# Kernel tuning notes

Measured on AMD Instinct MI355X. Metric: run time of the kernel, lower is better.

The kernel has to match this reference:

```python
import jax, jax.numpy as jnp
import numpy as np

KH, KW = 2, 2  # kernel_size; stride == kernel_size (default), pad == 0 for this config

def setup_inputs() -> dict:
    key = jax.random.key(0)
    k1, k2 = jax.random.split(key)
    B, C, H, W = 32, 64, 64, 64
    nH, nW = H // KH, W // KW
    L = nH * nW                     # 1024
    n = KH * KW * C                 # 256 (grouping = in_feature)
    x = jax.random.normal(k1, (B, C, H, W), dtype=jnp.float32)
    stdv = 6.0 / np.sqrt(n * n / 1.0) ** 0.5  # placeholder, recomputed below
    stdv = 6.0 / np.sqrt(float(n * n) / 1.0) if False else 6.0 / np.sqrt(float(n) * float(n) / float(n)) / 1.0
    stdv = 6.0 / np.sqrt(float(n * n))  # numel // L == n*n -> stdv = 6/sqrt(n*n) = 6/n
    weight = jax.random.uniform(k2, (L, n, n), dtype=jnp.float32, minval=-stdv, maxval=stdv)
    bias = jnp.zeros((1, 1, n, L), dtype=jnp.float32)
    return {"x": x, "weight": weight, "bias": bias}

def reference(x, weight, bias):
    # PointConv with kernel=(2,2), stride=(2,2), pad=0, grouping=C.
    B, C, H, W = x.shape
    nH, nW = H // KH, W // KW
    L = nH * nW
    n = C * KH * KW
    # F.unfold (non-overlapping, stride==kernel): channel order (c, kh, kw), L order (ph, pw)
    patches = x.reshape(B, C, nH, KH, nW, KW).transpose(0, 1, 3, 5, 2, 4).reshape(B, n, L)
    p = patches.reshape(B, 1, n, L)  # (B, C//grouping=1, n, L)
    # per-location matmul: distinct [n,n] weight per spatial patch l
    m = jnp.einsum('bcnl,lnp->bcpl', p, weight) + bias  # (B,1,n,L)
    m = m.reshape(B, C, KH, KW, nH, nW)
    # F.fold inverse of the unfold above
    out = m.transpose(0, 1, 4, 2, 5, 3).reshape(B, C, H, W)
    return out
```

## Files before the change

kernel.cpp:

```cpp
#include <hip/hip_runtime.h>


#define B_  32
#define C_  64
#define H_  64
#define W_  64
#define L_  1024
#define N_  256
#define SA  264
#define PW  268

typedef __bf16 bf16x8 __attribute__((ext_vector_type(8)));
typedef float  f32x4  __attribute__((ext_vector_type(4)));

__device__ __forceinline__ unsigned short f2bf(float f) {
  unsigned int u = __builtin_bit_cast(unsigned int, f);
  u += 0x7FFFu + ((u >> 16) & 1u);
  return (unsigned short)(u >> 16);
}

__global__ __launch_bounds__(256, 3) void pointconv_kernel(
    const float* __restrict__ x, const float* __restrict__ wgt,
    const float* __restrict__ bias, float* __restrict__ out) {
  __shared__ unsigned short A[B_ * SA];
  __shared__ unsigned short WS[32 * PW];

  const int bid = blockIdx.x;
  const int l  = ((bid & 7) << 7) | (bid >> 3);
  const int ph = l >> 5, pw = l & 31;
  const int h0 = ph * 2, w0 = pw * 2;
  const int tid = threadIdx.x;

  const float* __restrict__ wl = wgt + (size_t)l * (N_ * N_);

  const int kb = (tid >> 6) * 8;
  const int pq = (tid & 63) * 4;
  const float* wbase = wl + kb * N_ + pq;

  f32x4 wreg[8];
#pragma unroll
  for (int i = 0; i < 8; ++i)
    wreg[i] = *(const f32x4*)(wbase + i * N_);

  {
    const int b  = tid & 31;
    const int c0 = tid >> 5;
#pragma unroll
    for (int i = 0; i < 8; ++i) {
      const int c = c0 + i * 8;
      const float* px = x + (((b * C_ + c) * H_ + h0) * W_ + w0);
      float2 v0 = *(const float2*)px;
      float2 v1 = *(const float2*)(px + W_);
      ushort4 q;
      q.x = f2bf(v0.x); q.y = f2bf(v0.y);
      q.z = f2bf(v1.x); q.w = f2bf(v1.y);
      *(ushort4*)&A[b * SA + c * 4] = q;
    }
  }

  const int lane = tid & 63;
  const int wv   = tid >> 6;
  const int col  = lane & 15;
  const int quad = lane >> 4;

  f32x4 acc[2][4];
#pragma unroll
  for (int nt = 0; nt < 4; ++nt) {
    const int p = wv * 64 + nt * 16 + col;
    const float bv = bias[p * L_ + l];
#pragma unroll
    for (int mt = 0; mt < 2; ++mt) {
      acc[mt][nt][0] = bv; acc[mt][nt][1] = bv;
      acc[mt][nt][2] = bv; acc[mt][nt][3] = bv;
    }
  }

#pragma unroll 1
  for (int k0 = 0; k0 < N_; k0 += 32) {
#pragma unroll
    for (int i = 0; i < 8; ++i) {
      ushort4 q;
      q.x = f2bf(wreg[i][0]); q.y = f2bf(wreg[i][1]);
      q.z = f2bf(wreg[i][2]); q.w = f2bf(wreg[i][3]);
      *(ushort4*)&WS[(kb + i) * PW + pq] = q;
    }
    __syncthreads();

    if (k0 + 32 < N_) {
      const float* nb = wbase + (k0 + 32) * N_;
#pragma unroll
      for (int i = 0; i < 8; ++i)
        wreg[i] = *(const f32x4*)(nb + i * N_);
    }

    bf16x8 af[2];
#pragma unroll
    for (int mt = 0; mt < 2; ++mt)
      af[mt] = *(const bf16x8*)&A[(mt * 16 + col) * SA + k0 + quad * 8];

#pragma unroll
    for (int nt = 0; nt < 4; ++nt) {
      const int p = wv * 64 + nt * 16 + col;
      union { unsigned short s[8]; bf16x8 v; } bu;
#pragma unroll
      for (int j = 0; j < 8; ++j)
        bu.s[j] = WS[(quad * 8 + j) * PW + p];
#pragma unroll
      for (int mt = 0; mt < 2; ++mt)
        acc[mt][nt] = __builtin_amdgcn_mfma_f32_16x16x32_bf16(
            af[mt], bu.v, acc[mt][nt], 0, 0, 0);
    }
    __syncthreads();
  }

#pragma unroll
  for (int mt = 0; mt < 2; ++mt) {
#pragma unroll
    for (int nt = 0; nt < 4; ++nt) {
      const int p  = wv * 64 + nt * 16 + col;
      const int c  = p >> 2;
      const int kh = (p >> 1) & 1;
      const int kw = p & 1;
      float* po = out + (((c * H_) + h0 + kh) * W_ + w0 + kw);
#pragma unroll
      for (int r = 0; r < 4; ++r) {
        const int b = mt * 16 + quad * 4 + r;
        po[b * (C_ * H_ * W_)] = acc[mt][nt][r];
      }
    }
  }
}

extern "C" void kernel_launch(void* const* d_in, const int* in_sizes, int n_in,
                              void* d_out, int out_size, void* d_ws, size_t ws_size,
                              hipStream_t stream) {
  const float* x    = (const float*)d_in[0];
  const float* wgt  = (const float*)d_in[1];
  const float* bias = (const float*)d_in[2];
  float* out = (float*)d_out;
  pointconv_kernel<<<dim3(L_), dim3(256), 0, stream>>>(x, wgt, bias, out);
}
```

Before: 418.3 us.

## Load weight fragments directly into registers, dropping the shared-memory weight staging

Each lane now loads the weight elements it needs for its MFMA B fragment straight from global memory into registers, with a double-buffered register prefetch of the next K-slice. This removes the LDS weight tile, its bf16 store/load round trip, and the two barriers per K-step, and fully unrolls the K loop. The cost is scalar, strided 4-byte global loads (16-float runs per row instead of 128-bit vector loads) and many more live registers (64 floats of prefetch), which may hurt coalescing efficiency and occupancy under the 3-blocks launch bound.

```diff
diff --git a/kernel.cpp b/kernel.cpp
--- a/kernel.cpp
+++ b/kernel.cpp
@@ -8,7 +8,6 @@
 #define L_  1024
 #define N_  256
 #define SA  264
-#define PW  268
 
 typedef __bf16 bf16x8 __attribute__((ext_vector_type(8)));
 typedef float  f32x4  __attribute__((ext_vector_type(4)));
@@ -23,7 +22,6 @@
     const float* __restrict__ x, const float* __restrict__ wgt,
     const float* __restrict__ bias, float* __restrict__ out) {
   __shared__ unsigned short A[B_ * SA];
-  __shared__ unsigned short WS[32 * PW];
 
   const int bid = blockIdx.x;
   const int l  = ((bid & 7) << 7) | (bid >> 3);
@@ -33,14 +31,20 @@
 
   const float* __restrict__ wl = wgt + (size_t)l * (N_ * N_);
 
-  const int kb = (tid >> 6) * 8;
-  const int pq = (tid & 63) * 4;
-  const float* wbase = wl + kb * N_ + pq;
+  const int lane = tid & 63;
+  const int wv   = tid >> 6;
+  const int col  = lane & 15;
+  const int quad = lane >> 4;
 
-  f32x4 wreg[8];
+  const float* __restrict__ wp = wl + (quad * 8) * N_ + wv * 64 + col;
+
+  float rb0[4][8], rb1[4][8];
+
 #pragma unroll
-  for (int i = 0; i < 8; ++i)
-    wreg[i] = *(const f32x4*)(wbase + i * N_);
+  for (int nt = 0; nt < 4; ++nt)
+#pragma unroll
+    for (int j = 0; j < 8; ++j)
+      rb0[nt][j] = wp[j * N_ + nt * 16];
 
   {
     const int b  = tid & 31;
@@ -58,11 +62,6 @@
     }
   }
 
-  const int lane = tid & 63;
-  const int wv   = tid >> 6;
-  const int col  = lane & 15;
-  const int quad = lane >> 4;
-
   f32x4 acc[2][4];
 #pragma unroll
   for (int nt = 0; nt < 4; ++nt) {
@@ -75,42 +74,43 @@
     }
   }
 
-#pragma unroll 1
-  for (int k0 = 0; k0 < N_; k0 += 32) {
+  __syncthreads();
+
 #pragma unroll
-    for (int i = 0; i < 8; ++i) {
-      ushort4 q;
-      q.x = f2bf(wreg[i][0]); q.y = f2bf(wreg[i][1]);
-      q.z = f2bf(wreg[i][2]); q.w = f2bf(wreg[i][3]);
-      *(ushort4*)&WS[(kb + i) * PW + pq] = q;
-    }
-    __syncthreads();
-
-    if (k0 + 32 < N_) {
-      const float* nb = wbase + (k0 + 32) * N_;
+  for (int s = 0; s < 8; ++s) {
+    if (s < 7) {
+      const float* np = wp + (s + 1) * 32 * N_;
+      if (s & 1) {
 #pragma unroll
-      for (int i = 0; i < 8; ++i)
-        wreg[i] = *(const f32x4*)(nb + i * N_);
+        for (int nt = 0; nt < 4; ++nt)
+#pragma unroll
+          for (int j = 0; j < 8; ++j)
+            rb0[nt][j] = np[j * N_ + nt * 16];
+      } else {
+#pragma unroll
+        for (int nt = 0; nt < 4; ++nt)
+#pragma unroll
+          for (int j = 0; j < 8; ++j)
+            rb1[nt][j] = np[j * N_ + nt * 16];
+      }
     }
 
     bf16x8 af[2];
 #pragma unroll
     for (int mt = 0; mt < 2; ++mt)
-      af[mt] = *(const bf16x8*)&A[(mt * 16 + col) * SA + k0 + quad * 8];
+      af[mt] = *(const bf16x8*)&A[(mt * 16 + col) * SA + s * 32 + quad * 8];
 
 #pragma unroll
     for (int nt = 0; nt < 4; ++nt) {
-      const int p = wv * 64 + nt * 16 + col;
-      union { unsigned short s[8]; bf16x8 v; } bu;
+      union { unsigned short u[8]; bf16x8 v; } bu;
 #pragma unroll
       for (int j = 0; j < 8; ++j)
-        bu.s[j] = WS[(quad * 8 + j) * PW + p];
+        bu.u[j] = f2bf((s & 1) ? rb1[nt][j] : rb0[nt][j]);
 #pragma unroll
       for (int mt = 0; mt < 2; ++mt)
         acc[mt][nt] = __builtin_amdgcn_mfma_f32_16x16x32_bf16(
             af[mt], bu.v, acc[mt][nt], 0, 0, 0);
     }
-    __syncthreads();
   }
 
 #pragma unroll
```

Measured after the change: 438.3 us. 1.05x slower.
